# Optimization experiments

Measured on AMD Instinct MI355X. Metric: run time of the kernel, lower is better.

The kernel has to match this reference:

```python
import jax, jax.numpy as jnp
import numpy as np

LN_EPS = 1e-5
BN_EPS = 1e-5


def lstm_scan(x, Wih, Whh, b, reverse=False):
    # x: [T, B, D]; Wih: [4H, D]; Whh: [4H, H]; b: [4H]
    H = Whh.shape[1]
    xg = jnp.einsum('tbd,gd->tbg', x, Wih) + b  # [T, B, 4H]
    if reverse:
        xg = xg[::-1]

    def step(carry, g_x):
        h, c = carry
        g = g_x + h @ Whh.T
        i, f, gg, o = jnp.split(g, 4, axis=-1)
        c = jax.nn.sigmoid(f) * c + jax.nn.sigmoid(i) * jnp.tanh(gg)
        h = jax.nn.sigmoid(o) * jnp.tanh(c)
        return (h, c), h

    B = x.shape[1]
    h0 = jnp.zeros((B, H), x.dtype)
    _, hs = jax.lax.scan(step, (h0, h0), xg)
    if reverse:
        hs = hs[::-1]
    return hs  # [T, B, H]


def layernorm(x, g, b):
    mu = jnp.mean(x, axis=-1, keepdims=True)
    var = jnp.mean(jnp.square(x - mu), axis=-1, keepdims=True)
    return (x - mu) * jax.lax.rsqrt(var + LN_EPS) * g + b


def setup_inputs() -> dict:
    key = jax.random.key(0)
    ks = jax.random.split(key, 16)
    B, T, E, H = 256, 256, 128, 128
    H2 = 2 * H
    s = 0.1  # weight init scale
    return {
        'inp_embed': jax.random.normal(ks[0], (B, T, E), jnp.float32),
        'inp_last_idx': jax.random.randint(ks[1], (B,), 0, T, jnp.int64),
        'Wih_f': s * jax.random.normal(ks[2], (4 * H, E), jnp.float32),
        'Whh_f': s * jax.random.normal(ks[3], (4 * H, H), jnp.float32),
        'b_f': s * jax.random.normal(ks[4], (4 * H,), jnp.float32),
        'Wih_r': s * jax.random.normal(ks[5], (4 * H, E), jnp.float32),
        'Whh_r': s * jax.random.normal(ks[6], (4 * H, H), jnp.float32),
        'b_r': s * jax.random.normal(ks[7], (4 * H,), jnp.float32),
        'ln1_g': jnp.ones((H2,), jnp.float32),
        'ln1_b': jnp.zeros((H2,), jnp.float32),
        'W1ih': s * jax.random.normal(ks[8], (4 * H2, H2), jnp.float32),
        'W1hh': s * jax.random.normal(ks[9], (4 * H2, H2), jnp.float32),
        'b1': s * jax.random.normal(ks[10], (4 * H2,), jnp.float32),
        'ln2_g': jnp.ones((H2,), jnp.float32),
        'ln2_b': jnp.zeros((H2,), jnp.float32),
        'W2ih': s * jax.random.normal(ks[11], (4 * H2, H2), jnp.float32),
        'W2hh': s * jax.random.normal(ks[12], (4 * H2, H2), jnp.float32),
        'b2': s * jax.random.normal(ks[13], (4 * H2,), jnp.float32),
        'bn_g': jnp.ones((H2,), jnp.float32),
        'bn_b': jnp.zeros((H2,), jnp.float32),
    }


def reference(inp_embed, inp_last_idx, Wih_f, Whh_f, b_f, Wih_r, Whh_r, b_r,
              ln1_g, ln1_b, W1ih, W1hh, b1, ln2_g, ln2_b, W2ih, W2hh, b2,
              bn_g, bn_b):
    # eval mode: dropouts are identity, batchnorm uses running stats (mean=0, var=1)
    x = jnp.transpose(inp_embed, (1, 0, 2))  # [T, B, E]
    h_fwd = lstm_scan(x, Wih_f, Whh_f, b_f, reverse=False)
    h_bwd = lstm_scan(x, Wih_r, Whh_r, b_r, reverse=True)
    bilstm_out = jnp.concatenate([h_fwd, h_bwd], axis=-1)  # [T, B, 2H]
    bilstm_out = layernorm(bilstm_out, ln1_g, ln1_b)
    lstm_out = lstm_scan(bilstm_out, W1ih, W1hh, b1)
    lstm_out = layernorm(lstm_out + bilstm_out, ln2_g, ln2_b)
    lstm_out = lstm_scan(lstm_out, W2ih, W2hh, b2)  # [T, B, 2H]
    # gather last valid timestep per batch element
    gathered = lstm_out[inp_last_idx, jnp.arange(lstm_out.shape[1])]  # [B, 2H]
    y = (gathered * jax.lax.rsqrt(jnp.float32(1.0 + BN_EPS))) * bn_g + bn_b
    return jax.nn.relu(y)
```

## Files before the change

kernel.cpp:

```cpp
#include <hip/hip_runtime.h>
#include <cstdint>
#include <cstddef>

typedef unsigned short u16;
typedef unsigned long long u64;
typedef __attribute__((ext_vector_type(8))) short bf16x8;
typedef __attribute__((ext_vector_type(4))) float f32x4;
typedef __attribute__((ext_vector_type(4))) unsigned short u16x4;

#define DEV __device__ __forceinline__

DEV float bf2f(u16 h) { union { unsigned int u; float f; } x; x.u = ((unsigned int)h) << 16; return x.f; }
DEV u16 f2bf(float f) {
    union { float f; unsigned int u; } x; x.f = f;
    unsigned int u = x.u;
    return (u16)((u + 0x7fffu + ((u >> 16) & 1u)) >> 16);
}
DEV float fsig(float x)  { float e = __expf(-x);      return __builtin_amdgcn_rcpf(1.0f + e); }
DEV float ftanh(float x) { float e = __expf(2.0f * x); return 1.0f - 2.0f * __builtin_amdgcn_rcpf(e + 1.0f); }
DEV f32x4 mfma16(bf16x8 a, bf16x8 b, f32x4 c) {
    return __builtin_amdgcn_mfma_f32_16x16x32_bf16(a, b, c, 0, 0, 0);
}


union __align__(16) SMemU {
    struct { u16 As[2][64][40]; u16 Bs[256][40]; } g;
    struct { u16 Al[2][16][136]; } r1;
    struct { u16 Al[16][264]; } r2;
};

__global__ __launch_bounds__(256) void prep_w4_kernel(
    const float* __restrict__ a0, u16* __restrict__ o0, int c0,
    const float* __restrict__ a1, u16* __restrict__ o1, int c1,
    const float* __restrict__ a2, u16* __restrict__ o2, int c2,
    const float* __restrict__ a3, u16* __restrict__ o3)
{
    int blk = blockIdx.x;
    const float* a; u16* o; int off;
    if (blk < c0)                { a = a0; o = o0; off = blk; }
    else if (blk < c0 + c1)      { a = a1; o = o1; off = blk - c0; }
    else if (blk < c0 + c1 + c2) { a = a2; o = o2; off = blk - c0 - c1; }
    else                         { a = a3; o = o3; off = blk - c0 - c1 - c2; }
    int i = off * 256 + threadIdx.x;
    o[i] = f2bf(a[i]);
}

__global__ __launch_bounds__(256) void prep_x1_kernel(
    float* __restrict__ X, const float* __restrict__ gw, const float* __restrict__ bw)
{
    int row  = blockIdx.x * 4 + (threadIdx.x >> 6);
    int lane = threadIdx.x & 63;
    float* xr = X + (size_t)row * 256;
    f32x4 v = *(const f32x4*)(xr + lane * 4);
    float s = v[0] + v[1] + v[2] + v[3];
    #pragma unroll
    for (int mm = 1; mm < 64; mm <<= 1) s += __shfl_xor(s, mm, 64);
    float mu = s * (1.0f / 256.0f);
    f32x4 e = v - mu;
    float q = e[0]*e[0] + e[1]*e[1] + e[2]*e[2] + e[3]*e[3];
    #pragma unroll
    for (int mm = 1; mm < 64; mm <<= 1) q += __shfl_xor(q, mm, 64);
    float rs = rsqrtf(q * (1.0f / 256.0f) + 1e-5f);
    int c0 = lane * 4;
    u16x4 hv, lv;
    #pragma unroll
    for (int i = 0; i < 4; ++i) {
        float o = e[i] * rs * gw[c0 + i] + bw[c0 + i];
        u16 hh = f2bf(o);
        hv[i] = hh;
        lv[i] = f2bf(o - bf2f(hh));
    }
    u16* H = (u16*)xr;
    *(u16x4*)(H + lane * 4)       = hv;
    *(u16x4*)(H + 256 + lane * 4) = lv;
}

DEV void xg_fr_body(SMemU* smu, int bx, int by, int nby,
    const float* __restrict__ embed,
    const u16* __restrict__ Wf16, const float* __restrict__ bf_,
    const u16* __restrict__ Wr16, const float* __restrict__ br_,
    float* __restrict__ xgf, float* __restrict__ xgr, int t0f, int t0r)
{
    auto& As = smu->g.As[0];
    auto& Bs = smu->g.Bs;
    int tid = threadIdx.x;
    int half = nby >> 1;
    bool isR = by >= half;
    int m0 = (by - (isR ? half : 0)) * 64;
    const u16* W      = isR ? Wr16 : Wf16;
    const float* bias = isR ? br_ : bf_;
    float* out        = isR ? xgr : xgf;
    int tbase         = isR ? t0r : t0f;
    int n0 = bx * 64;

    int r  = tid >> 2;
    int kc = (tid & 3) * 8;
    int m  = m0 + r;
    int tl = m >> 8, bb = m & 255;
    const float* arow = embed + ((size_t)(bb * 256 + (tbase + tl)) * 128);
    const u16* brow = W + ((size_t)(n0 + r) * 128);

    f32x4 acc[4];
    #pragma unroll
    for (int i = 0; i < 4; ++i) acc[i] = (f32x4){0.f, 0.f, 0.f, 0.f};
    int lane = tid & 63, w = tid >> 6;
    int fr_ = lane & 15, kb0 = (lane >> 4) * 8;

    for (int kt = 0; kt < 8; ++kt) {
        int sc = (kt & 3) * 32 + kc;
        bool lo = kt >= 4;
        f32x4 va = *(const f32x4*)(arow + sc);
        f32x4 vb = *(const f32x4*)(arow + sc + 4);
        bf16x8 wv = *(const bf16x8*)(brow + sc);
        bf16x8 hv;
        #pragma unroll
        for (int i = 0; i < 8; ++i) {
            float v = (i < 4) ? va[i] : vb[i - 4];
            u16 hi = f2bf(v);
            hv[i] = (short)(lo ? f2bf(v - bf2f(hi)) : hi);
        }
        *(bf16x8*)&As[r][kc] = hv;
        *(bf16x8*)&Bs[r][kc] = wv;
        __syncthreads();
        bf16x8 bfrg = *(const bf16x8*)&Bs[w * 16 + fr_][kb0];
        #pragma unroll
        for (int mt = 0; mt < 4; ++mt) {
            bf16x8 afrg = *(const bf16x8*)&As[mt * 16 + fr_][kb0];
            acc[mt] = mfma16(afrg, bfrg, acc[mt]);
        }
        __syncthreads();
    }
    int col = n0 + w * 16 + fr_;
    float bvv = bias[col];
    int rq = (lane >> 4) * 4;
    #pragma unroll
    for (int mt = 0; mt < 4; ++mt)
        #pragma unroll
        for (int rr = 0; rr < 4; ++rr) {
            int mrow = m0 + mt * 16 + rq + rr;
            out[(size_t)mrow * 512 + col] = acc[mt][rr] + bvv;
        }
}

DEV void xg_l16_body(SMemU* smu, int bx, int by,
    const u16* __restrict__ X1p, const u16* __restrict__ Wp,
    const float* __restrict__ bias, float* __restrict__ out, int t0)
{
    auto& As = smu->g.As;
    auto& Bs = smu->g.Bs;
    int tid = threadIdx.x;
    int m0 = by * 64, n0 = bx * 256;
    int rA = tid >> 2, kcA = (tid & 3) * 8;
    int m  = m0 + rA;
    int tl = m >> 8, bb = m & 255;
    const u16* arow = X1p + ((size_t)((t0 + tl) * 256 + bb)) * 512;
    const u16* brow = Wp + ((size_t)(n0 + tid)) * 256;
    int swB = (tid >> 3) & 3;

    f32x4 acc[4][4];
    #pragma unroll
    for (int cs = 0; cs < 4; ++cs)
        #pragma unroll
        for (int i = 0; i < 4; ++i) acc[cs][i] = (f32x4){0.f, 0.f, 0.f, 0.f};
    int lane = tid & 63, w = tid >> 6;
    int fr_ = lane & 15, quad = lane >> 4, kb0 = quad * 8;

    for (int kt = 0; kt < 8; ++kt) {
        int sc = kt * 32;
        bf16x8 hvH = *(const bf16x8*)(arow + sc + kcA);
        bf16x8 hvL = *(const bf16x8*)(arow + 256 + sc + kcA);
        bf16x8 wv0 = *(const bf16x8*)(brow + sc);
        bf16x8 wv1 = *(const bf16x8*)(brow + sc + 8);
        bf16x8 wv2 = *(const bf16x8*)(brow + sc + 16);
        bf16x8 wv3 = *(const bf16x8*)(brow + sc + 24);
        *(bf16x8*)&As[0][rA][kcA] = hvH;
        *(bf16x8*)&As[1][rA][kcA] = hvL;
        *(bf16x8*)&Bs[tid][(0 ^ swB) * 8] = wv0;
        *(bf16x8*)&Bs[tid][(1 ^ swB) * 8] = wv1;
        *(bf16x8*)&Bs[tid][(2 ^ swB) * 8] = wv2;
        *(bf16x8*)&Bs[tid][(3 ^ swB) * 8] = wv3;
        __syncthreads();
        bf16x8 bfrg[4];
        #pragma unroll
        for (int cs = 0; cs < 4; ++cs) {
            int Br = cs * 64 + w * 16 + fr_;
            int g  = quad ^ ((Br >> 3) & 3);
            bfrg[cs] = *(const bf16x8*)&Bs[Br][g * 8];
        }
        #pragma unroll
        for (int h = 0; h < 2; ++h)
            #pragma unroll
            for (int mt = 0; mt < 4; ++mt) {
                bf16x8 afrg = *(const bf16x8*)&As[h][mt * 16 + fr_][kb0];
                #pragma unroll
                for (int cs = 0; cs < 4; ++cs)
                    acc[cs][mt] = mfma16(afrg, bfrg[cs], acc[cs][mt]);
            }
        __syncthreads();
    }
    int rq = (lane >> 4) * 4;
    #pragma unroll
    for (int cs = 0; cs < 4; ++cs) {
        int col = n0 + cs * 64 + w * 16 + fr_;
        float bvv = bias[col];
        #pragma unroll
        for (int mt = 0; mt < 4; ++mt)
            #pragma unroll
            for (int rr = 0; rr < 4; ++rr) {
                int mrow = m0 + mt * 16 + rq + rr;
                out[(size_t)mrow * 1024 + col] = acc[cs][mt][rr] + bvv;
            }
    }
}

DEV void xg_ln3_body(SMemU* smu, int bx, int by,
    const u16* __restrict__ X1p, const float* __restrict__ Rc,
    const float* __restrict__ l2g, const float* __restrict__ l2b,
    const u16* __restrict__ Wp, const float* __restrict__ bias,
    float* __restrict__ out, int t0)
{
    auto& As = smu->g.As;
    auto& Bs = smu->g.Bs;
    int tid = threadIdx.x;
    int m0 = by * 64, n0 = bx * 128;
    int rA = tid >> 2, kcA = (tid & 3) * 8;
    int rB = tid >> 1, cB = tid & 1;
    int m  = m0 + rA;
    int tl = m >> 8, bb = m & 255;
    const u16* a1 = X1p + ((size_t)((t0 + tl) * 256 + bb)) * 512;
    const float* a2 = Rc + ((size_t)(tl * 256 + bb)) * 256;
    const u16* brow = Wp + ((size_t)(n0 + rB)) * 256;
    int swB = (rB >> 3) & 3;

    float xc[8][8];
    float s = 0.f;
    #pragma unroll
    for (int q = 0; q < 8; ++q) {
        int sc = q * 32 + kcA;
        bf16x8 hx = *(const bf16x8*)(a1 + sc);
        bf16x8 lx = *(const bf16x8*)(a1 + 256 + sc);
        f32x4 u2 = *(const f32x4*)(a2 + sc);
        f32x4 v2 = *(const f32x4*)(a2 + sc + 4);
        #pragma unroll
        for (int i = 0; i < 8; ++i) {
            float rv = (i < 4) ? u2[i] : v2[i - 4];
            xc[q][i] = bf2f((u16)hx[i]) + bf2f((u16)lx[i]) + rv;
            s += xc[q][i];
        }
    }
    s += __shfl_xor(s, 1); s += __shfl_xor(s, 2);
    float mu = s * (1.0f / 256.0f);
    float q2 = 0.f;
    #pragma unroll
    for (int q = 0; q < 8; ++q)
        #pragma unroll
        for (int i = 0; i < 8; ++i) { float e = xc[q][i] - mu; q2 += e * e; }
    q2 += __shfl_xor(q2, 1); q2 += __shfl_xor(q2, 2);
    float rs = rsqrtf(q2 * (1.0f / 256.0f) + 1e-5f);
    #pragma unroll
    for (int q = 0; q < 8; ++q) {
        int sc = q * 32 + kcA;
        f32x4 g1 = *(const f32x4*)(l2g + sc);
        f32x4 g2v = *(const f32x4*)(l2g + sc + 4);
        f32x4 h1 = *(const f32x4*)(l2b + sc);
        f32x4 h2 = *(const f32x4*)(l2b + sc + 4);
        #pragma unroll
        for (int i = 0; i < 4; ++i) {
            xc[q][i]     = (xc[q][i]     - mu) * rs * g1[i]  + h1[i];
            xc[q][4 + i] = (xc[q][4 + i] - mu) * rs * g2v[i] + h2[i];
        }
    }

    f32x4 acc[2][4];
    #pragma unroll
    for (int cs = 0; cs < 2; ++cs)
        #pragma unroll
        for (int i = 0; i < 4; ++i) acc[cs][i] = (f32x4){0.f, 0.f, 0.f, 0.f};
    int lane = tid & 63, w = tid >> 6;
    int fr_ = lane & 15, quad = lane >> 4, kb0 = quad * 8;

    #pragma unroll
    for (int kt = 0; kt < 8; ++kt) {
        int sc = kt * 32;
        bf16x8 wv0 = *(const bf16x8*)(brow + sc + cB * 16);
        bf16x8 wv1 = *(const bf16x8*)(brow + sc + cB * 16 + 8);
        bf16x8 hvH, hvL;
        #pragma unroll
        for (int i = 0; i < 8; ++i) {
            float v = xc[kt][i];
            u16 hi = f2bf(v);
            hvH[i] = (short)hi;
            hvL[i] = (short)f2bf(v - bf2f(hi));
        }
        *(bf16x8*)&As[0][rA][kcA] = hvH;
        *(bf16x8*)&As[1][rA][kcA] = hvL;
        *(bf16x8*)&Bs[rB][((2 * cB) ^ swB) * 8]     = wv0;
        *(bf16x8*)&Bs[rB][((2 * cB + 1) ^ swB) * 8] = wv1;
        __syncthreads();
        bf16x8 bfrg[2];
        #pragma unroll
        for (int cs = 0; cs < 2; ++cs) {
            int Br = cs * 64 + w * 16 + fr_;
            int g  = quad ^ ((Br >> 3) & 3);
            bfrg[cs] = *(const bf16x8*)&Bs[Br][g * 8];
        }
        #pragma unroll
        for (int h = 0; h < 2; ++h)
            #pragma unroll
            for (int mt = 0; mt < 4; ++mt) {
                bf16x8 afrg = *(const bf16x8*)&As[h][mt * 16 + fr_][kb0];
                #pragma unroll
                for (int cs = 0; cs < 2; ++cs)
                    acc[cs][mt] = mfma16(afrg, bfrg[cs], acc[cs][mt]);
            }
        __syncthreads();
    }
    int rq = (lane >> 4) * 4;
    #pragma unroll
    for (int cs = 0; cs < 2; ++cs) {
        int col = n0 + cs * 64 + w * 16 + fr_;
        float bvv = bias[col];
        #pragma unroll
        for (int mt = 0; mt < 4; ++mt)
            #pragma unroll
            for (int rr = 0; rr < 4; ++rr) {
                int mrow = m0 + mt * 16 + rq + rr;
                out[(size_t)mrow * 1024 + col] = acc[cs][mt][rr] + bvv;
            }
    }
}

DEV void recur1_body(SMemU* smu, int bid,
    const float* __restrict__ xgf, const float* __restrict__ xgr,
    const u16* __restrict__ whf16, const u16* __restrict__ whr16,
    float* __restrict__ cbf, float* __restrict__ cbr,
    float* __restrict__ hpf, float* __restrict__ hpr,
    float* __restrict__ xout, int s0, int s1)
{
    __builtin_amdgcn_s_setprio(1);
    constexpr int K = 128, N4 = 512;
    auto& Al = smu->r1.Al;

    int tid = threadIdx.x, lane = tid & 63, w = tid >> 6;
    int fr_ = lane & 15, quad = lane >> 4, kb0 = quad * 8;
    int dir = bid >> 5, gidx = bid & 31;
    const float* xg  = dir ? xgr  : xgf;
    const u16* whh16 = dir ? whr16 : whf16;
    float* cb = dir ? cbr : cbf;
    float* hp = dir ? hpr : hpf;
    int coloff = dir ? 128 : 0;

    bf16x8 bf[4][2][4];
    #pragma unroll
    for (int g = 0; g < 4; ++g)
        #pragma unroll
        for (int u = 0; u < 2; ++u) {
            const u16* src = whh16 + (size_t)(g * K + w * 32 + u * 16 + fr_) * K;
            #pragma unroll
            for (int kt = 0; kt < 4; ++kt)
                bf[g][u][kt] = *(const bf16x8*)(src + kt * 32 + kb0);
        }

    int uq = quad >> 1, qrow = quad & 1;
    int colw = w * 32 + uq * 16 + fr_;
    int b0 = gidx * 8;
    float c[4];
    #pragma unroll
    for (int rr = 0; rr < 4; ++rr)
        c[rr] = (s0 > 0) ? cb[(size_t)(b0 + qrow * 4 + rr) * K + colw] : 0.f;

    if (s0 > 0) {
        for (int idx = tid; idx < 8 * K; idx += 256) {
            int sa = idx >> 7, k = idx & 127;
            float v = hp[(size_t)(b0 + sa) * K + k];
            u16 hh = f2bf(v);
            Al[s0 & 1][sa][k] = hh;
            Al[s0 & 1][8 + sa][k] = f2bf(v - bf2f(hh));
        }
    }
    __syncthreads();

    float xv[4][4];
    {
        int xrow = dir ? (s1 - 1 - s0) : 0;
        #pragma unroll
        for (int rr = 0; rr < 4; ++rr) {
            const float* xp = xg + ((size_t)(xrow * 256 + b0 + qrow * 4 + rr)) * N4 + colw;
            #pragma unroll
            for (int g = 0; g < 4; ++g) xv[rr][g] = xp[g * K];
        }
    }

    for (int t = s0; t < s1; ++t) {
        float xn[4][4];
        {
            int tn = (t + 1 < s1) ? (t + 1) : t;
            int xrow = dir ? (s1 - 1 - tn) : (tn - s0);
            #pragma unroll
            for (int rr = 0; rr < 4; ++rr) {
                const float* xp = xg + ((size_t)(xrow * 256 + b0 + qrow * 4 + rr)) * N4 + colw;
                #pragma unroll
                for (int g = 0; g < 4; ++g) xn[rr][g] = xp[g * K];
            }
        }
        f32x4 acc[4][2];
        if (t > 0) {
            #pragma unroll
            for (int g = 0; g < 4; ++g)
                #pragma unroll
                for (int u = 0; u < 2; ++u) acc[g][u] = (f32x4){0.f, 0.f, 0.f, 0.f};
            #pragma unroll
            for (int kt = 0; kt < 4; ++kt) {
                bf16x8 a = *(const bf16x8*)&Al[t & 1][fr_][kt * 32 + kb0];
                #pragma unroll
                for (int g = 0; g < 4; ++g)
                    #pragma unroll
                    for (int u = 0; u < 2; ++u) acc[g][u] = mfma16(a, bf[g][u][kt], acc[g][u]);
            }
            #pragma unroll
            for (int g = 0; g < 4; ++g)
                #pragma unroll
                for (int u = 0; u < 2; ++u)
                    #pragma unroll
                    for (int rr = 0; rr < 4; ++rr)
                        acc[g][u][rr] += __shfl_xor(acc[g][u][rr], 32);
        }
        int tt = dir ? (255 - t) : t;
        #pragma unroll
        for (int rr = 0; rr < 4; ++rr) {
            int s = qrow * 4 + rr;
            float gg[4];
            #pragma unroll
            for (int g = 0; g < 4; ++g) {
                float pv = (t > 0) ? (uq ? acc[g][1][rr] : acc[g][0][rr]) : 0.f;
                gg[g] = xv[rr][g] + pv;
            }
            c[rr] = fsig(gg[1]) * c[rr] + fsig(gg[0]) * ftanh(gg[2]);
            float h = fsig(gg[3]) * ftanh(c[rr]);
            u16 hh = f2bf(h);
            Al[(t + 1) & 1][s][colw] = hh;
            Al[(t + 1) & 1][8 + s][colw] = f2bf(h - bf2f(hh));
            xout[((size_t)tt * 256 + b0 + s) * 256 + coloff + colw] = h;
            if (t == s1 - 1) hp[(size_t)(b0 + s) * K + colw] = h;
        }
        __syncthreads();
        #pragma unroll
        for (int rr = 0; rr < 4; ++rr)
            #pragma unroll
            for (int g = 0; g < 4; ++g) xv[rr][g] = xn[rr][g];
    }
    #pragma unroll
    for (int rr = 0; rr < 4; ++rr)
        cb[(size_t)(b0 + qrow * 4 + rr) * K + colw] = c[rr];
}

template<int OUTY>
DEV void recur2_body(SMemU* smu, int bid,
    const float* __restrict__ xg, const u16* __restrict__ whh16,
    float* __restrict__ cb, u64* hb,
    float* __restrict__ xoutc, float* __restrict__ yout,
    const int* __restrict__ lastidx,
    const float* __restrict__ bng, const float* __restrict__ bnb,
    int s0, int s1)
{
    __builtin_amdgcn_s_setprio(1);
    constexpr int K = 256, MB = 8, N4 = 1024;
    constexpr int CNT = MB * K / 256;
    auto& Al = smu->r2.Al;

    int tid = threadIdx.x, lane = tid & 63, w = tid >> 6;
    int fr_ = lane & 15, quad = lane >> 4, kb0 = quad * 8;
    int group = bid >> 2, cw = bid & 3;
    u64* hbg = hb + (size_t)group * (2 * MB * K);
    int col = cw * 64 + w * 16 + fr_;

    bf16x8 bf[4][8];
    #pragma unroll
    for (int g = 0; g < 4; ++g) {
        const u16* src = whh16 + (size_t)(g * 256 + col) * K;
        #pragma unroll
        for (int kt = 0; kt < 8; ++kt)
            bf[g][kt] = *(const bf16x8*)(src + kt * 32 + kb0);
    }

    int qrow = quad & 1, rhalf = quad >> 1;
    int sp[2], bs[2]; float c[2];
    #pragma unroll
    for (int j = 0; j < 2; ++j) {
        sp[j] = qrow * 4 + rhalf * 2 + j;
        bs[j] = group * 8 + sp[j];
        c[j] = (s0 > 0) ? cb[(size_t)bs[j] * K + col] : 0.f;
    }
    int lastb[2] = { -1, -1 };
    float bngv = 0.f, bnbv = 0.f;
    if (OUTY) {
        bool is64 = (lastidx[1] | lastidx[3] | lastidx[5] | lastidx[7] |
                     lastidx[9] | lastidx[11] | lastidx[13] | lastidx[15]) == 0;
        lastb[0] = is64 ? lastidx[2 * bs[0]] : lastidx[bs[0]];
        lastb[1] = is64 ? lastidx[2 * bs[1]] : lastidx[bs[1]];
        bngv = bng[col] * rsqrtf(1.0f + 1e-5f);
        bnbv = bnb[col];
    }

    float xv[2][4];
    #pragma unroll
    for (int j = 0; j < 2; ++j) {
        const float* xp = xg + ((size_t)bs[j]) * N4 + col;
        #pragma unroll
        for (int g = 0; g < 4; ++g) xv[j][g] = xp[g * 256];
    }

    for (int t = s0; t < s1; ++t) {
        float xn[2][4];
        {
            int tn = (t + 1 < s1) ? (t + 1) : t;
            int xr = tn - s0;
            #pragma unroll
            for (int j = 0; j < 2; ++j) {
                const float* xp = xg + ((size_t)(xr * 256 + bs[j])) * N4 + col;
                #pragma unroll
                for (int g = 0; g < 4; ++g) xn[j][g] = xp[g * 256];
            }
        }
        f32x4 acc[4];
        if (t > 0) {
            u64* hsrc = hbg + (size_t)(t & 1) * (MB * K);
            u64 v[CNT];
            #pragma unroll
            for (int i = 0; i < CNT; ++i)
                v[i] = __hip_atomic_load(hsrc + tid + i * 256,
                                         __ATOMIC_RELAXED, __HIP_MEMORY_SCOPE_AGENT);
            for (;;) {
                bool ok = true;
                #pragma unroll
                for (int i = 0; i < CNT; ++i)
                    if ((unsigned int)(v[i] >> 32) != (unsigned int)t) ok = false;
                if (ok) break;
                __builtin_amdgcn_s_sleep(1);
                #pragma unroll
                for (int i = 0; i < CNT; ++i)
                    if ((unsigned int)(v[i] >> 32) != (unsigned int)t)
                        v[i] = __hip_atomic_load(hsrc + tid + i * 256,
                                                 __ATOMIC_RELAXED, __HIP_MEMORY_SCOPE_AGENT);
            }
            #pragma unroll
            for (int i = 0; i < CNT; ++i) {
                unsigned int d = (unsigned int)v[i];
                Al[i][tid]     = (u16)(d & 0xffffu);
                Al[8 + i][tid] = (u16)(d >> 16);
            }
            __syncthreads();
            #pragma unroll
            for (int g = 0; g < 4; ++g) acc[g] = (f32x4){0.f, 0.f, 0.f, 0.f};
            #pragma unroll
            for (int kt = 0; kt < 8; ++kt) {
                bf16x8 a = *(const bf16x8*)&Al[fr_][kt * 32 + kb0];
                #pragma unroll
                for (int g = 0; g < 4; ++g) acc[g] = mfma16(a, bf[g][kt], acc[g]);
            }
            #pragma unroll
            for (int g = 0; g < 4; ++g)
                #pragma unroll
                for (int rr = 0; rr < 4; ++rr)
                    acc[g][rr] += __shfl_xor(acc[g][rr], 32);
        }
        #pragma unroll
        for (int j = 0; j < 2; ++j) {
            float gg[4];
            #pragma unroll
            for (int g = 0; g < 4; ++g) {
                float pv = (t > 0) ? (rhalf ? acc[g][2 + j] : acc[g][j]) : 0.f;
                gg[g] = xv[j][g] + pv;
            }
            c[j] = fsig(gg[1]) * c[j] + fsig(gg[0]) * ftanh(gg[2]);
            float h = fsig(gg[3]) * ftanh(c[j]);
            u16 hh = f2bf(h);
            u16 hl = f2bf(h - bf2f(hh));
            u64 word = (u64)((unsigned int)hh | ((unsigned int)hl << 16))
                     | ((u64)(unsigned int)(t + 1) << 32);
            __hip_atomic_store(hbg + (size_t)((t + 1) & 1) * (MB * K) + (size_t)sp[j] * K + col,
                               word, __ATOMIC_RELAXED, __HIP_MEMORY_SCOPE_AGENT);
            if (OUTY == 0) {
                xoutc[((size_t)(t - s0) * 256 + bs[j]) * 256 + col] = h;
            } else if (t == lastb[j]) {
                float y = h * bngv + bnbv;
                y = y > 0.f ? y : 0.f;
                yout[(size_t)bs[j] * 256 + col] = y;
            }
        }
        #pragma unroll
        for (int j = 0; j < 2; ++j)
            #pragma unroll
            for (int g = 0; g < 4; ++g) xv[j][g] = xn[j][g];
    }
    #pragma unroll
    for (int j = 0; j < 2; ++j) cb[(size_t)bs[j] * K + col] = c[j];
}

__global__ __launch_bounds__(256) void fused1_kernel(
    const float* __restrict__ embed,
    const u16* __restrict__ Wf16, const float* __restrict__ bfb,
    const u16* __restrict__ Wr16, const float* __restrict__ brb,
    float* __restrict__ xgfw, float* __restrict__ xgrw, int t0f, int t0r, int gon,
    const float* __restrict__ xgfr, const float* __restrict__ xgrr,
    const u16* __restrict__ whf16, const u16* __restrict__ whr16,
    float* __restrict__ cbf, float* __restrict__ cbr,
    float* __restrict__ hpf, float* __restrict__ hpr,
    float* __restrict__ X1, int s0, int s1, int ron)
{
    __shared__ SMemU sm;
    int b = blockIdx.x;
    if (b < 64) {
        if (ron)
            recur1_body(&sm, b, xgfr, xgrr, whf16, whr16, cbf, cbr, hpf, hpr, X1, s0, s1);
    } else {
        if (gon) {
            int idx = b - 64;
            xg_fr_body(&sm, idx & 7, idx >> 3, 256, embed, Wf16, bfb, Wr16, brb,
                       xgfw, xgrw, t0f, t0r);
        }
    }
}

__global__ __launch_bounds__(256) void fused2_kernel(
    const float* __restrict__ xg2, const u16* __restrict__ wh1,
    float* __restrict__ cb1, u64* hb1, float* __restrict__ Rw,
    int s2a, int s2b, int s2on,
    const float* __restrict__ xg3, const u16* __restrict__ wh2,
    float* __restrict__ cb2, u64* hb2, float* __restrict__ yout,
    const int* __restrict__ lastidx, const float* __restrict__ bng,
    const float* __restrict__ bnb, int s3a, int s3b, int s3on,
    const u16* __restrict__ X1p, const u16* __restrict__ w1p,
    const float* __restrict__ b1, float* __restrict__ G2w, int g2t0, int g2on,
    const float* __restrict__ Rr, const float* __restrict__ ln2g,
    const float* __restrict__ ln2b, const u16* __restrict__ w2p,
    const float* __restrict__ b2v, float* __restrict__ G3w, int g3t0, int g3on)
{
    __shared__ SMemU sm;
    int b = blockIdx.x;
    if (b < 256) {
        int x = b & 7, k = b >> 3;
        int sub = k & 15;
        int gid = (x * 4 + (sub >> 2)) * 4 + (sub & 3);
        if (k < 16) {
            if (s2on)
                recur2_body<0>(&sm, gid, xg2, wh1, cb1, hb1, Rw,
                               nullptr, nullptr, nullptr, nullptr, s2a, s2b);
        } else {
            if (s3on)
                recur2_body<1>(&sm, gid, xg3, wh2, cb2, hb2,
                               nullptr, yout, lastidx, bng, bnb, s3a, s3b);
        }
    } else if (b < 512) {
        if (g2on) {
            int i = b - 256;
            xg_l16_body(&sm, i & 3, i >> 2, X1p, w1p, b1, G2w, g2t0);
        }
    } else {
        if (g3on) {
            int i = b - 512;
            xg_ln3_body(&sm, i & 7, i >> 3, X1p, Rr, ln2g, ln2b, w2p, b2v, G3w, g3t0);
        }
    }
}

__global__ __launch_bounds__(256) void xg2_kernel(
    const u16* __restrict__ X1p, const u16* __restrict__ Wp,
    const float* __restrict__ bias, float* __restrict__ out, int t0)
{
    __shared__ SMemU sm;
    xg_l16_body(&sm, blockIdx.x, blockIdx.y, X1p, Wp, bias, out, t0);
}

extern "C" void kernel_launch(void* const* d_in, const int* in_sizes, int n_in,
                              void* d_out, int out_size, void* d_ws, size_t ws_size,
                              hipStream_t stream)
{
    (void)in_sizes; (void)n_in; (void)out_size; (void)ws_size;
    const float* embed = (const float*)d_in[0];
    const int* lastidx = (const int*)d_in[1];
    const float* Wih_f = (const float*)d_in[2];
    const float* Whh_f = (const float*)d_in[3];
    const float* b_f   = (const float*)d_in[4];
    const float* Wih_r = (const float*)d_in[5];
    const float* Whh_r = (const float*)d_in[6];
    const float* b_r   = (const float*)d_in[7];
    const float* ln1g  = (const float*)d_in[8];
    const float* ln1b  = (const float*)d_in[9];
    const float* W1ih  = (const float*)d_in[10];
    const float* W1hh  = (const float*)d_in[11];
    const float* b1    = (const float*)d_in[12];
    const float* ln2g  = (const float*)d_in[13];
    const float* ln2b  = (const float*)d_in[14];
    const float* W2ih  = (const float*)d_in[15];
    const float* W2hh  = (const float*)d_in[16];
    const float* b2    = (const float*)d_in[17];
    const float* bng   = (const float*)d_in[18];
    const float* bnb   = (const float*)d_in[19];

    const size_t MiB = 1024 * 1024;
    char* ws = (char*)d_ws;
    float* G2[2] = { (float*)ws,               (float*)(ws + 16 * MiB) };
    float* G3[2] = { (float*)(ws + 32 * MiB),  (float*)(ws + 48 * MiB) };
    float* X1    =   (float*)(ws + 64 * MiB);
    float* R[2]  = { (float*)(ws + 128 * MiB), (float*)(ws + 132 * MiB) };
    char* p = ws + 136 * MiB;
    u64* hb1 = (u64*)p;                         p += 1024 * 1024;
    u64* hb2 = (u64*)p;                         p += 1024 * 1024;
    float* cbf = (float*)p;                     p += 128 * 1024;
    float* cbr = (float*)p;                     p += 128 * 1024;
    float* cb1 = (float*)p;                     p += 256 * 1024;
    float* cb2 = (float*)p;                     p += 256 * 1024;
    float* hpf = (float*)p;                     p += 128 * 1024;
    float* hpr = (float*)p;                     p += 128 * 1024;
    u16* w1p   = (u16*)p;                       p += 512 * 1024;
    u16* w2p   = (u16*)p;                       p += 512 * 1024;
    u16* wfp   = (u16*)p;                       p += 128 * 1024;
    u16* wrp   = (u16*)p;                       p += 128 * 1024;
    u16* wh1p  = (u16*)p;                       p += 512 * 1024;
    u16* wh2p  = (u16*)p;                       p += 512 * 1024;
    u16* whfp  = (u16*)p;                       p += 128 * 1024;
    u16* whrp  = (u16*)p;

    const int CH1 = 32, n1 = 8;
    const int CH  = 16, n2 = 16;

    prep_w4_kernel<<<2560, 256, 0, stream>>>(
        W1ih, w1p, 1024, W2ih, w2p, 1024, Wih_f, wfp, 256, Wih_r, wrp);
    prep_w4_kernel<<<2560, 256, 0, stream>>>(
        W1hh, wh1p, 1024, W2hh, wh2p, 1024, Whh_f, whfp, 256, Whh_r, whrp);

    for (int i = 0; i <= n1; ++i) {
        int gon = (i < n1), ron = (i >= 1);
        float* wf = (i & 1) ? G3[0] : G2[0];
        float* wr = (i & 1) ? G3[1] : G2[1];
        const float* rf = ((i - 1) & 1) ? G3[0] : G2[0];
        const float* rr_ = ((i - 1) & 1) ? G3[1] : G2[1];
        fused1_kernel<<<2112, 256, 0, stream>>>(
            embed, wfp, b_f, wrp, b_r, wf, wr, CH1 * i, 256 - CH1 * (i + 1), gon,
            rf, rr_, whfp, whrp, cbf, cbr, hpf, hpr, X1, CH1 * (i - 1), CH1 * i, ron);
    }

    prep_x1_kernel<<<16384, 256, 0, stream>>>(X1, ln1g, ln1b);
    const u16* X1p = (const u16*)X1;

    xg2_kernel<<<dim3(4, CH * 4), 256, 0, stream>>>(X1p, w1p, b1, G2[0], 0);
    for (int i = 0; i <= n2 + 1; ++i) {
        int s2on = (i < n2), s3on = (i >= 2);
        int g2on = (i + 1 < n2), g3on = (i >= 1 && i <= n2);
        fused2_kernel<<<1024, 256, 0, stream>>>(
            G2[i & 1], wh1p, cb1, hb1, R[i & 1], CH * i, CH * (i + 1), s2on,
            G3[(i - 2) & 1], wh2p, cb2, hb2, (float*)d_out, lastidx, bng, bnb,
            CH * (i - 2), CH * (i - 1), s3on,
            X1p, w1p, b1, G2[(i + 1) & 1], CH * (i + 1), g2on,
            R[(i - 1) & 1], ln2g, ln2b, w2p, b2, G3[(i - 1) & 1], CH * (i - 1), g3on);
    }
}
```

Baseline: 1.886 ms.

## Replace per-chunk fused2 launches with one persistent kernel synchronised by flags

The layer-2/3 stage used to be 18 kernel launches, with the cell state saved to and reloaded from global memory at each chunk boundary. It is now one persistent kernel. 256 blocks run the two recurrent chains, keeping the cell state in registers, and 256 worker blocks compute the input-gate projections chunk by chunk. Progress is signalled through global atomic counters with acquire/release semantics. This removes launch gaps and the state round-trips, but it relies on all 512 blocks being co-resident and adds spin-wait overhead.

```diff
diff --git a/kernel.cpp b/kernel.cpp
--- a/kernel.cpp
+++ b/kernel.cpp
@@ -3,6 +3,7 @@
 #include <cstddef>
 
 typedef unsigned short u16;
+typedef unsigned int u32;
 typedef unsigned long long u64;
 typedef __attribute__((ext_vector_type(8))) short bf16x8;
 typedef __attribute__((ext_vector_type(4))) float f32x4;
@@ -28,6 +29,23 @@
     struct { u16 Al[2][16][136]; } r1;
     struct { u16 Al[16][264]; } r2;
 };
+
+enum { G2D = 0, G3D = 32, C2F = 64, C3F = 96 };
+
+template<int SLP>
+DEV void wflag(u32* p, u32 tgt) {
+    if (threadIdx.x == 0) {
+        while (__hip_atomic_load(p, __ATOMIC_RELAXED, __HIP_MEMORY_SCOPE_AGENT) < tgt)
+            __builtin_amdgcn_s_sleep(SLP);
+        __hip_atomic_fetch_add(p, 0u, __ATOMIC_ACQUIRE, __HIP_MEMORY_SCOPE_AGENT);
+    }
+    __syncthreads();
+}
+DEV void sflag(u32* p, u32 v) {
+    __syncthreads();
+    if (threadIdx.x == 0)
+        __hip_atomic_fetch_add(p, v, __ATOMIC_RELEASE, __HIP_MEMORY_SCOPE_AGENT);
+}
 
 __global__ __launch_bounds__(256) void prep_w4_kernel(
     const float* __restrict__ a0, u16* __restrict__ o0, int c0,
@@ -455,13 +473,13 @@
 }
 
 template<int OUTY>
-DEV void recur2_body(SMemU* smu, int bid,
-    const float* __restrict__ xg, const u16* __restrict__ whh16,
-    float* __restrict__ cb, u64* hb,
-    float* __restrict__ xoutc, float* __restrict__ yout,
-    const int* __restrict__ lastidx,
+DEV void pchain_body(SMemU* smu, int bid,
+    const float* __restrict__ xga, const float* __restrict__ xgb,
+    const u16* __restrict__ whh16, u64* hb,
+    float* __restrict__ r0, float* __restrict__ r1,
+    float* __restrict__ yout, const int* __restrict__ lastidx,
     const float* __restrict__ bng, const float* __restrict__ bnb,
-    int s0, int s1)
+    u32* fl)
 {
     __builtin_amdgcn_s_setprio(1);
     constexpr int K = 256, MB = 8, N4 = 1024;
@@ -484,12 +502,11 @@
     }
 
     int qrow = quad & 1, rhalf = quad >> 1;
-    int sp[2], bs[2]; float c[2];
+    int sp[2], bs[2]; float c[2] = {0.f, 0.f};
     #pragma unroll
     for (int j = 0; j < 2; ++j) {
         sp[j] = qrow * 4 + rhalf * 2 + j;
         bs[j] = group * 8 + sp[j];
-        c[j] = (s0 > 0) ? cb[(size_t)bs[j] * K + col] : 0.f;
     }
     int lastb[2] = { -1, -1 };
     float bngv = 0.f, bnbv = 0.f;
@@ -502,99 +519,169 @@
         bnbv = bnb[col];
     }
 
-    float xv[2][4];
-    #pragma unroll
-    for (int j = 0; j < 2; ++j) {
-        const float* xp = xg + ((size_t)bs[j]) * N4 + col;
-        #pragma unroll
-        for (int g = 0; g < 4; ++g) xv[j][g] = xp[g * 256];
-    }
-
-    for (int t = s0; t < s1; ++t) {
-        float xn[2][4];
-        {
-            int tn = (t + 1 < s1) ? (t + 1) : t;
-            int xr = tn - s0;
+    for (int ch = 0; ch < 16; ++ch) {
+        if (OUTY == 0) {
+            wflag<8>(fl + G2D + ch, 256);
+            if (ch >= 2) wflag<8>(fl + G3D + ch - 2, 512);
+        } else {
+            wflag<8>(fl + G3D + ch, 512);
+        }
+        const float* xg = (ch & 1) ? xgb : xga;
+        float* Rw = (ch & 1) ? r1 : r0;
+
+        float xv[2][4];
+        #pragma unroll
+        for (int j = 0; j < 2; ++j) {
+            const float* xp = xg + ((size_t)bs[j]) * N4 + col;
+            #pragma unroll
+            for (int g = 0; g < 4; ++g) xv[j][g] = xp[g * 256];
+        }
+
+        for (int tt = 0; tt < 16; ++tt) {
+            int t = ch * 16 + tt;
+            float xn[2][4];
+            {
+                int xr = (tt + 1 < 16) ? (tt + 1) : tt;
+                #pragma unroll
+                for (int j = 0; j < 2; ++j) {
+                    const float* xp = xg + ((size_t)(xr * 256 + bs[j])) * N4 + col;
+                    #pragma unroll
+                    for (int g = 0; g < 4; ++g) xn[j][g] = xp[g * 256];
+                }
+            }
+            f32x4 acc[4];
+            if (t > 0) {
+                u64* hsrc = hbg + (size_t)(t & 1) * (MB * K);
+                u64 v[CNT];
+                #pragma unroll
+                for (int i = 0; i < CNT; ++i)
+                    v[i] = __hip_atomic_load(hsrc + tid + i * 256,
+                                             __ATOMIC_RELAXED, __HIP_MEMORY_SCOPE_AGENT);
+                for (;;) {
+                    bool ok = true;
+                    #pragma unroll
+                    for (int i = 0; i < CNT; ++i)
+                        if ((unsigned int)(v[i] >> 32) != (unsigned int)t) ok = false;
+                    if (ok) break;
+                    __builtin_amdgcn_s_sleep(1);
+                    #pragma unroll
+                    for (int i = 0; i < CNT; ++i)
+                        if ((unsigned int)(v[i] >> 32) != (unsigned int)t)
+                            v[i] = __hip_atomic_load(hsrc + tid + i * 256,
+                                                     __ATOMIC_RELAXED, __HIP_MEMORY_SCOPE_AGENT);
+                }
+                #pragma unroll
+                for (int i = 0; i < CNT; ++i) {
+                    unsigned int d = (unsigned int)v[i];
+                    Al[i][tid]     = (u16)(d & 0xffffu);
+                    Al[8 + i][tid] = (u16)(d >> 16);
+                }
+                __syncthreads();
+                #pragma unroll
+                for (int g = 0; g < 4; ++g) acc[g] = (f32x4){0.f, 0.f, 0.f, 0.f};
+                #pragma unroll
+                for (int kt = 0; kt < 8; ++kt) {
+                    bf16x8 a = *(const bf16x8*)&Al[fr_][kt * 32 + kb0];
+                    #pragma unroll
+                    for (int g = 0; g < 4; ++g) acc[g] = mfma16(a, bf[g][kt], acc[g]);
+                }
+                #pragma unroll
+                for (int g = 0; g < 4; ++g)
+                    #pragma unroll
+                    for (int rr = 0; rr < 4; ++rr)
+                        acc[g][rr] += __shfl_xor(acc[g][rr], 32);
+            }
             #pragma unroll
             for (int j = 0; j < 2; ++j) {
-                const float* xp = xg + ((size_t)(xr * 256 + bs[j])) * N4 + col;
-                #pragma unroll
-                for (int g = 0; g < 4; ++g) xn[j][g] = xp[g * 256];
-            }
-        }
-        f32x4 acc[4];
-        if (t > 0) {
-            u64* hsrc = hbg + (size_t)(t & 1) * (MB * K);
-            u64 v[CNT];
-            #pragma unroll
-            for (int i = 0; i < CNT; ++i)
-                v[i] = __hip_atomic_load(hsrc + tid + i * 256,
-                                         __ATOMIC_RELAXED, __HIP_MEMORY_SCOPE_AGENT);
-            for (;;) {
-                bool ok = true;
-                #pragma unroll
-                for (int i = 0; i < CNT; ++i)
-                    if ((unsigned int)(v[i] >> 32) != (unsigned int)t) ok = false;
-                if (ok) break;
-                __builtin_amdgcn_s_sleep(1);
-                #pragma unroll
-                for (int i = 0; i < CNT; ++i)
-                    if ((unsigned int)(v[i] >> 32) != (unsigned int)t)
-                        v[i] = __hip_atomic_load(hsrc + tid + i * 256,
-                                                 __ATOMIC_RELAXED, __HIP_MEMORY_SCOPE_AGENT);
-            }
-            #pragma unroll
-            for (int i = 0; i < CNT; ++i) {
-                unsigned int d = (unsigned int)v[i];
-                Al[i][tid]     = (u16)(d & 0xffffu);
-                Al[8 + i][tid] = (u16)(d >> 16);
+                float gg[4];
+                #pragma unroll
+                for (int g = 0; g < 4; ++g) {
+                    float pv = (t > 0) ? (rhalf ? acc[g][2 + j] : acc[g][j]) : 0.f;
+                    gg[g] = xv[j][g] + pv;
+                }
+                c[j] = fsig(gg[1]) * c[j] + fsig(gg[0]) * ftanh(gg[2]);
+                float h = fsig(gg[3]) * ftanh(c[j]);
+                u16 hh = f2bf(h);
+                u16 hl = f2bf(h - bf2f(hh));
+                u64 word = (u64)((unsigned int)hh | ((unsigned int)hl << 16))
+                         | ((u64)(unsigned int)(t + 1) << 32);
+                __hip_atomic_store(hbg + (size_t)((t + 1) & 1) * (MB * K) + (size_t)sp[j] * K + col,
+                                   word, __ATOMIC_RELAXED, __HIP_MEMORY_SCOPE_AGENT);
+                if (OUTY == 0) {
+                    Rw[((size_t)tt * 256 + bs[j]) * 256 + col] = h;
+                } else if (t == lastb[j]) {
+                    float y = h * bngv + bnbv;
+                    y = y > 0.f ? y : 0.f;
+                    yout[(size_t)bs[j] * 256 + col] = y;
+                }
             }
             __syncthreads();
             #pragma unroll
-            for (int g = 0; g < 4; ++g) acc[g] = (f32x4){0.f, 0.f, 0.f, 0.f};
-            #pragma unroll
-            for (int kt = 0; kt < 8; ++kt) {
-                bf16x8 a = *(const bf16x8*)&Al[fr_][kt * 32 + kb0];
-                #pragma unroll
-                for (int g = 0; g < 4; ++g) acc[g] = mfma16(a, bf[g][kt], acc[g]);
-            }
-            #pragma unroll
-            for (int g = 0; g < 4; ++g)
-                #pragma unroll
-                for (int rr = 0; rr < 4; ++rr)
-                    acc[g][rr] += __shfl_xor(acc[g][rr], 32);
-        }
-        #pragma unroll
-        for (int j = 0; j < 2; ++j) {
-            float gg[4];
-            #pragma unroll
-            for (int g = 0; g < 4; ++g) {
-                float pv = (t > 0) ? (rhalf ? acc[g][2 + j] : acc[g][j]) : 0.f;
-                gg[g] = xv[j][g] + pv;
-            }
-            c[j] = fsig(gg[1]) * c[j] + fsig(gg[0]) * ftanh(gg[2]);
-            float h = fsig(gg[3]) * ftanh(c[j]);
-            u16 hh = f2bf(h);
-            u16 hl = f2bf(h - bf2f(hh));
-            u64 word = (u64)((unsigned int)hh | ((unsigned int)hl << 16))
-                     | ((u64)(unsigned int)(t + 1) << 32);
-            __hip_atomic_store(hbg + (size_t)((t + 1) & 1) * (MB * K) + (size_t)sp[j] * K + col,
-                               word, __ATOMIC_RELAXED, __HIP_MEMORY_SCOPE_AGENT);
-            if (OUTY == 0) {
-                xoutc[((size_t)(t - s0) * 256 + bs[j]) * 256 + col] = h;
-            } else if (t == lastb[j]) {
-                float y = h * bngv + bnbv;
-                y = y > 0.f ? y : 0.f;
-                yout[(size_t)bs[j] * 256 + col] = y;
-            }
-        }
-        #pragma unroll
-        for (int j = 0; j < 2; ++j)
-            #pragma unroll
-            for (int g = 0; g < 4; ++g) xv[j][g] = xn[j][g];
-    }
-    #pragma unroll
-    for (int j = 0; j < 2; ++j) cb[(size_t)bs[j] * K + col] = c[j];
+            for (int j = 0; j < 2; ++j)
+                #pragma unroll
+                for (int g = 0; g < 4; ++g) xv[j][g] = xn[j][g];
+        }
+        sflag(fl + (OUTY ? C3F : C2F) + ch, 1);
+    }
+}
+
+DEV void pworker_body(SMemU* smu, int wid,
+    const u16* __restrict__ X1p, const u16* __restrict__ w1p,
+    const float* __restrict__ b1, float* g2a, float* g2b,
+    const float* r0, const float* r1,
+    const float* __restrict__ ln2g, const float* __restrict__ ln2b,
+    const u16* __restrict__ w2p, const float* __restrict__ b2v,
+    float* g3a, float* g3b, u32* fl)
+{
+    for (int c = 0; c <= 16; ++c) {
+        if (c < 16) {
+            if (c >= 2) wflag<32>(fl + C2F + c - 2, 128);
+            xg_l16_body(smu, wid & 3, wid >> 2, X1p, w1p, b1,
+                        (c & 1) ? g2b : g2a, 16 * c);
+            sflag(fl + G2D + c, 1);
+        }
+        if (c >= 1) {
+            int cc = c - 1;
+            wflag<32>(fl + C2F + cc, 128);
+            if (cc >= 2) wflag<32>(fl + C3F + cc - 2, 128);
+            const float* Rr = (cc & 1) ? r1 : r0;
+            float* g3 = (cc & 1) ? g3b : g3a;
+            int i0 = wid * 2, i1 = wid * 2 + 1;
+            xg_ln3_body(smu, i0 & 7, i0 >> 3, X1p, Rr, ln2g, ln2b, w2p, b2v, g3, 16 * cc);
+            xg_ln3_body(smu, i1 & 7, i1 >> 3, X1p, Rr, ln2g, ln2b, w2p, b2v, g3, 16 * cc);
+            sflag(fl + G3D + cc, 2);
+        }
+    }
+}
+
+__global__ __launch_bounds__(256, 2) void persist_kernel(
+    float* g2a, float* g2b, float* g3a, float* g3b,
+    const u16* __restrict__ wh1, const u16* __restrict__ wh2,
+    u64* hb1, u64* hb2, float* r0, float* r1,
+    float* __restrict__ yout, const int* __restrict__ lastidx,
+    const float* __restrict__ bng, const float* __restrict__ bnb,
+    const u16* __restrict__ X1p, const u16* __restrict__ w1p,
+    const float* __restrict__ b1,
+    const float* __restrict__ ln2g, const float* __restrict__ ln2b,
+    const u16* __restrict__ w2p, const float* __restrict__ b2v,
+    u32* fl)
+{
+    __shared__ SMemU sm;
+    int b = blockIdx.x;
+    if (b < 256) {
+        int x = b & 7, k = b >> 3;
+        int sub = k & 15;
+        int gid = (x * 4 + (sub >> 2)) * 4 + (sub & 3);
+        if (k < 16)
+            pchain_body<0>(&sm, gid, g2a, g2b, wh1, hb1, r0, r1,
+                           nullptr, nullptr, nullptr, nullptr, fl);
+        else
+            pchain_body<1>(&sm, gid, g3a, g3b, wh2, hb2, nullptr, nullptr,
+                           yout, lastidx, bng, bnb, fl);
+    } else {
+        pworker_body(&sm, b - 256, X1p, w1p, b1, g2a, g2b, r0, r1,
+                     ln2g, ln2b, w2p, b2v, g3a, g3b, fl);
+    }
 }
 
 __global__ __launch_bounds__(256) void fused1_kernel(
@@ -620,56 +707,6 @@
                        xgfw, xgrw, t0f, t0r);
         }
     }
-}
-
-__global__ __launch_bounds__(256) void fused2_kernel(
-    const float* __restrict__ xg2, const u16* __restrict__ wh1,
-    float* __restrict__ cb1, u64* hb1, float* __restrict__ Rw,
-    int s2a, int s2b, int s2on,
-    const float* __restrict__ xg3, const u16* __restrict__ wh2,
-    float* __restrict__ cb2, u64* hb2, float* __restrict__ yout,
-    const int* __restrict__ lastidx, const float* __restrict__ bng,
-    const float* __restrict__ bnb, int s3a, int s3b, int s3on,
-    const u16* __restrict__ X1p, const u16* __restrict__ w1p,
-    const float* __restrict__ b1, float* __restrict__ G2w, int g2t0, int g2on,
-    const float* __restrict__ Rr, const float* __restrict__ ln2g,
-    const float* __restrict__ ln2b, const u16* __restrict__ w2p,
-    const float* __restrict__ b2v, float* __restrict__ G3w, int g3t0, int g3on)
-{
-    __shared__ SMemU sm;
-    int b = blockIdx.x;
-    if (b < 256) {
-        int x = b & 7, k = b >> 3;
-        int sub = k & 15;
-        int gid = (x * 4 + (sub >> 2)) * 4 + (sub & 3);
-        if (k < 16) {
-            if (s2on)
-                recur2_body<0>(&sm, gid, xg2, wh1, cb1, hb1, Rw,
-                               nullptr, nullptr, nullptr, nullptr, s2a, s2b);
-        } else {
-            if (s3on)
-                recur2_body<1>(&sm, gid, xg3, wh2, cb2, hb2,
-                               nullptr, yout, lastidx, bng, bnb, s3a, s3b);
-        }
-    } else if (b < 512) {
-        if (g2on) {
-            int i = b - 256;
-            xg_l16_body(&sm, i & 3, i >> 2, X1p, w1p, b1, G2w, g2t0);
-        }
-    } else {
-        if (g3on) {
-            int i = b - 512;
-            xg_ln3_body(&sm, i & 7, i >> 3, X1p, Rr, ln2g, ln2b, w2p, b2v, G3w, g3t0);
-        }
-    }
-}
-
-__global__ __launch_bounds__(256) void xg2_kernel(
-    const u16* __restrict__ X1p, const u16* __restrict__ Wp,
-    const float* __restrict__ bias, float* __restrict__ out, int t0)
-{
-    __shared__ SMemU sm;
-    xg_l16_body(&sm, blockIdx.x, blockIdx.y, X1p, Wp, bias, out, t0);
 }
 
 extern "C" void kernel_launch(void* const* d_in, const int* in_sizes, int n_in,
@@ -709,8 +746,6 @@
     u64* hb2 = (u64*)p;                         p += 1024 * 1024;
     float* cbf = (float*)p;                     p += 128 * 1024;
     float* cbr = (float*)p;                     p += 128 * 1024;
-    float* cb1 = (float*)p;                     p += 256 * 1024;
-    float* cb2 = (float*)p;                     p += 256 * 1024;
     float* hpf = (float*)p;                     p += 128 * 1024;
     float* hpr = (float*)p;                     p += 128 * 1024;
     u16* w1p   = (u16*)p;                       p += 512 * 1024;
@@ -720,10 +755,12 @@
     u16* wh1p  = (u16*)p;                       p += 512 * 1024;
     u16* wh2p  = (u16*)p;                       p += 512 * 1024;
     u16* whfp  = (u16*)p;                       p += 128 * 1024;
-    u16* whrp  = (u16*)p;
+    u16* whrp  = (u16*)p;                       p += 128 * 1024;
+    u32* fl    = (u32*)p;
 
     const int CH1 = 32, n1 = 8;
-    const int CH  = 16, n2 = 16;
+
+    hipMemsetAsync(fl, 0, 4096, stream);
 
     prep_w4_kernel<<<2560, 256, 0, stream>>>(
         W1ih, w1p, 1024, W2ih, w2p, 1024, Wih_f, wfp, 256, Wih_r, wrp);
@@ -744,15 +781,8 @@
     prep_x1_kernel<<<16384, 256, 0, stream>>>(X1, ln1g, ln1b);
     const u16* X1p = (const u16*)X1;
 
-    xg2_kernel<<<dim3(4, CH * 4), 256, 0, stream>>>(X1p, w1p, b1, G2[0], 0);
-    for (int i = 0; i <= n2 + 1; ++i) {
-        int s2on = (i < n2), s3on = (i >= 2);
-        int g2on = (i + 1 < n2), g3on = (i >= 1 && i <= n2);
-        fused2_kernel<<<1024, 256, 0, stream>>>(
-            G2[i & 1], wh1p, cb1, hb1, R[i & 1], CH * i, CH * (i + 1), s2on,
-            G3[(i - 2) & 1], wh2p, cb2, hb2, (float*)d_out, lastidx, bng, bnb,
-            CH * (i - 2), CH * (i - 1), s3on,
-            X1p, w1p, b1, G2[(i + 1) & 1], CH * (i + 1), g2on,
-            R[(i - 1) & 1], ln2g, ln2b, w2p, b2, G3[(i - 1) & 1], CH * (i - 1), g3on);
-    }
-}
+    persist_kernel<<<512, 256, 0, stream>>>(
+        G2[0], G2[1], G3[0], G3[1], wh1p, wh2p, hb1, hb2, R[0], R[1],
+        (float*)d_out, lastidx, bng, bnb,
+        X1p, w1p, b1, ln2g, ln2b, w2p, b2, fl);
+}
```

New measurement: 2.526 ms. +33.9%, slower.
